# Optimization experiments

Hardware: AMD Instinct MI355X
Metric: run time of the kernel (lower is better)

The kernel has to match this reference:

```python
import jax, jax.numpy as jnp
import numpy as np

# CODABlocks (codomain attention) with per_channel_attention=True:
# token_codimension = head_codimension = 1, scale = 2, n_modes = [32, 32],
# mixer_modes = [16, 16], temperature = 1.0, instance_norm (affine) everywhere.
N_HEADS = 16
TEMPERATURE = 1.0
EPS = 1e-5

def _gelu(z):
    return jax.nn.gelu(z, approximate=False)  # matches torch F.gelu default (erf)

def instance_norm(x, g, b):
    # x: (B, C, H, W); normalize over spatial dims per (sample, channel), affine.
    mu = jnp.mean(x, axis=(-2, -1), keepdims=True)
    var = jnp.var(x, axis=(-2, -1), keepdims=True)
    return (x - mu) * jax.lax.rsqrt(var + EPS) * g[:, None, None] + b[:, None, None]

def conv1x1(x, w, b):
    return jnp.einsum('bihw,io->bohw', x, w) + b[None, :, None, None]

def fourier_resample(x, out_shape):
    # FFT-based spatial resampling (mode truncation / zero-pad), norm='forward'.
    if tuple(x.shape[-2:]) == tuple(out_shape):
        return x
    Ho, Wo = out_shape
    xft = jnp.fft.rfftn(x, axes=(-2, -1), norm='forward')
    out = jnp.zeros(x.shape[:-2] + (Ho, Wo // 2 + 1), dtype=xft.dtype)
    hk = min(x.shape[-2], Ho) // 2
    wk = min(xft.shape[-1], Wo // 2 + 1)
    out = out.at[..., :hk, :wk].set(xft[..., :hk, :wk])
    out = out.at[..., -hk:, :wk].set(xft[..., -hk:, :wk])
    return jnp.fft.irfftn(out, s=out_shape, axes=(-2, -1), norm='forward')

def spectral_conv(x, w, out_shape):
    # Truncated-mode spectral convolution (dense weights, equiv. to tucker rank=1.0).
    # w: (Cin, Cout, 2*mh, mw, 2) -> complex weight on kept Fourier modes.
    wc = w[..., 0] + 1j * w[..., 1]
    mh = wc.shape[2] // 2
    mw = wc.shape[3]
    Ho, Wo = out_shape
    xft = jnp.fft.rfftn(x, axes=(-2, -1), norm='forward')   # (B, Cin, H, W//2+1)
    top = jnp.einsum('bihw,iohw->bohw', xft[:, :, :mh, :mw], wc[:, :, :mh])
    bot = jnp.einsum('bihw,iohw->bohw', xft[:, :, -mh:, :mw], wc[:, :, mh:])
    out_ft = jnp.zeros((x.shape[0], wc.shape[1], Ho, Wo // 2 + 1), dtype=xft.dtype)
    out_ft = out_ft.at[:, :, :mh, :mw].set(top)
    out_ft = out_ft.at[:, :, -mh:, :mw].set(bot)
    return jnp.fft.irfftn(out_ft, s=out_shape, axes=(-2, -1), norm='forward')

def fno_layer(x, spec_w, skip_w, skip_b, out_shape, norm=None, act=None):
    # One FNOBlocks layer: spectral conv + (resampled) linear skip, optional norm/act.
    xs = fourier_resample(conv1x1(x, skip_w, skip_b), out_shape)
    xf = spectral_conv(x, spec_w, out_shape)
    if norm is not None:
        xf = instance_norm(xf, *norm)
    y = xf + xs
    return act(y) if act is not None else y

def codano_forward(x, key_w, key_skip_w, key_skip_b, query_w, query_skip_w, query_skip_b, value_w, value_skip_w, value_skip_b, proj_w, proj_skip_w, proj_skip_b, norm1_g, norm1_b, attn_norm_g, attn_norm_b, norm2_g, norm2_b, mixer_w1, mixer_skip_w1, mixer_skip_b1, mixer_norm_g1, mixer_norm_b1, mixer_w2, mixer_skip_w2, mixer_skip_b2, mixer_norm_g2, mixer_norm_b2, mixer_out_g, mixer_out_b):
    b, t, H, W = x.shape   # token codim d = 1 -> channel dim == number of tokens
    tokens = x.reshape(b * t, 1, H, W)
    tokens_norm = instance_norm(tokens, norm1_g, norm1_b)
    Hs, Ws = H // 2, W // 2   # K, Q downsampled by scale = 2
    k = fno_layer(tokens_norm, key_w, key_skip_w, key_skip_b, (Hs, Ws))
    q = fno_layer(tokens_norm, query_w, query_skip_w, query_skip_b, (Hs, Ws))
    v = fno_layer(tokens_norm, value_w, value_skip_w, value_skip_b, (H, W))

    def heads_flat(z):
        hh, ww = z.shape[-2:]
        # (b*t, n_heads*d, h, w) -> (b, heads, t, d*h*w), d = 1
        return z.reshape(b, t, N_HEADS, hh * ww).transpose(0, 2, 1, 3)

    kf, qf, vf = heads_flat(k), heads_flat(q), heads_flat(v)
    scale = jnp.sqrt(jnp.asarray(kf.shape[-1], jnp.float32)) * TEMPERATURE
    dprod = jax.nn.softmax(jnp.einsum('bhtd,bhsd->bhts', qf, kf) / scale, axis=-1)
    attn = jnp.einsum('bhts,bhsd->bhtd', dprod, vf)      # (b, heads, t, H*W)
    attn = attn.transpose(0, 2, 1, 3).reshape(b * t, N_HEADS, H, W)
    # multi-head projection back to token codimension (n_heads -> 1)
    attn = fno_layer(attn, proj_w, proj_skip_w, proj_skip_b, (H, W))
    attn = instance_norm(attn + tokens, attn_norm_g, attn_norm_b)
    # permutation-equivariant mixer: 2 FNO layers shared across all tokens
    m = instance_norm(attn, norm2_g, norm2_b)
    m = fno_layer(m, mixer_w1, mixer_skip_w1, mixer_skip_b1, (H, W), norm=(mixer_norm_g1, mixer_norm_b1), act=_gelu)
    m = fno_layer(m, mixer_w2, mixer_skip_w2, mixer_skip_b2, (H, W), norm=(mixer_norm_g2, mixer_norm_b2))
    out = instance_norm(m, mixer_out_g, mixer_out_b) + attn
    return out.reshape(b, t, H, W)

def setup_inputs():
    key = jax.random.key(0)
    ks = list(jax.random.split(key, 32))
    f32 = jnp.float32
    def W_(k, shape, s=0.02):
        return (s * jax.random.normal(k, shape)).astype(f32)
    B, T, H, Wd = 4, 32, 128, 128
    mh_s, mw_s = 16, 9    # mixer_modes [16,16]: 2*(16//2) rows, 16//2+1 rfft cols
    mh_f, mw_f = 32, 17   # n_modes [32,32]
    return {
        'x': jax.random.normal(ks[0], (B, T, H, Wd), dtype=f32),
        'key_w': W_(ks[1], (1, N_HEADS, mh_s, mw_s, 2)),
        'key_skip_w': W_(ks[2], (1, N_HEADS), 0.5),
        'key_skip_b': W_(ks[3], (N_HEADS,)),
        'query_w': W_(ks[4], (1, N_HEADS, mh_s, mw_s, 2)),
        'query_skip_w': W_(ks[5], (1, N_HEADS), 0.5),
        'query_skip_b': W_(ks[6], (N_HEADS,)),
        'value_w': W_(ks[7], (1, N_HEADS, mh_s, mw_s, 2)),
        'value_skip_w': W_(ks[8], (1, N_HEADS), 0.5),
        'value_skip_b': W_(ks[9], (N_HEADS,)),
        'proj_w': W_(ks[10], (N_HEADS, 1, mh_f, mw_f, 2)),
        'proj_skip_w': W_(ks[11], (N_HEADS, 1), 0.25),
        'proj_skip_b': W_(ks[12], (1,)),
        'norm1_g': jnp.ones((1,), f32), 'norm1_b': jnp.zeros((1,), f32),
        'attn_norm_g': jnp.ones((1,), f32), 'attn_norm_b': jnp.zeros((1,), f32),
        'norm2_g': jnp.ones((1,), f32), 'norm2_b': jnp.zeros((1,), f32),
        'mixer_w1': W_(ks[13], (1, 1, mh_f, mw_f, 2)),
        'mixer_skip_w1': W_(ks[14], (1, 1), 0.5),
        'mixer_skip_b1': W_(ks[15], (1,)),
        'mixer_norm_g1': jnp.ones((1,), f32), 'mixer_norm_b1': jnp.zeros((1,), f32),
        'mixer_w2': W_(ks[16], (1, 1, mh_f, mw_f, 2)),
        'mixer_skip_w2': W_(ks[17], (1, 1), 0.5),
        'mixer_skip_b2': W_(ks[18], (1,)),
        'mixer_norm_g2': jnp.ones((1,), f32), 'mixer_norm_b2': jnp.zeros((1,), f32),
        'mixer_out_g': jnp.ones((1,), f32), 'mixer_out_b': jnp.zeros((1,), f32),
    }

def reference(x, key_w, key_skip_w, key_skip_b, query_w, query_skip_w, query_skip_b, value_w, value_skip_w, value_skip_b, proj_w, proj_skip_w, proj_skip_b, norm1_g, norm1_b, attn_norm_g, attn_norm_b, norm2_g, norm2_b, mixer_w1, mixer_skip_w1, mixer_skip_b1, mixer_norm_g1, mixer_norm_b1, mixer_w2, mixer_skip_w2, mixer_skip_b2, mixer_norm_g2, mixer_norm_b2, mixer_out_g, mixer_out_b):
    return codano_forward(x, key_w, key_skip_w, key_skip_b, query_w, query_skip_w, query_skip_b, value_w, value_skip_w, value_skip_b, proj_w, proj_skip_w, proj_skip_b, norm1_g, norm1_b, attn_norm_g, attn_norm_b, norm2_g, norm2_b, mixer_w1, mixer_skip_w1, mixer_skip_b1, mixer_norm_g1, mixer_norm_b1, mixer_w2, mixer_skip_w2, mixer_skip_b2, mixer_norm_g2, mixer_norm_b2, mixer_out_g, mixer_out_b)
```

## Files before the change

### kernel.cpp

```cpp
#include <hip/hip_runtime.h>
#include <cmath>

#define PI_F 3.14159265358979323846f
#define NTOK 128
#define NPIX 16384
#define NHEADS 16

__device__ __forceinline__ void block_reduce2(float& a, float& b){
  __shared__ float sa[4], sb[4];
  __syncthreads();
  for (int o=32;o>0;o>>=1){ a += __shfl_down(a,o); b += __shfl_down(b,o); }
  int w = threadIdx.x>>6, l = threadIdx.x&63;
  if (l==0){ sa[w]=a; sb[w]=b; }
  __syncthreads();
  a = sa[0]+sa[1]+sa[2]+sa[3];
  b = sb[0]+sb[1]+sb[2]+sb[3];
}

__device__ __forceinline__ float block_reduce1(float a){
  __shared__ float sa[4];
  __syncthreads();
  for (int o=32;o>0;o>>=1) a += __shfl_down(a,o);
  int w = threadIdx.x>>6, l = threadIdx.x&63;
  if (l==0) sa[w]=a;
  __syncthreads();
  return sa[0]+sa[1]+sa[2]+sa[3];
}

__device__ __forceinline__ float gelu_f(float y){
  return 0.5f*y*(1.f + erff(y*0.70710678118f));
}

__device__ __forceinline__ void affine_from(const float* __restrict__ ps, float g, float bb, int t,
                                            float& a, float& b0){
  float sum=0.f,sq=0.f;
  #pragma unroll
  for (int s=0;s<8;s++){ const float* p=ps+((size_t)t*8+s)*2; sum+=p[0]; sq+=p[1]; }
  const float iN=1.f/NPIX;
  float mu=sum*iN, var=sq*iN-mu*mu;
  a=rsqrtf(var+1e-5f)*g;
  b0=bb-mu*a;
}
__device__ __forceinline__ void scalA_from(const float* __restrict__ psA, float ag, float n2g, int t,
                                           float& muZ, float& aA, float& a0){
  float sum=0.f,sq=0.f;
  #pragma unroll
  for (int s=0;s<16;s++){ const float* p=psA+((size_t)t*16+s)*2; sum+=p[0]; sq+=p[1]; }
  const float iN=1.f/NPIX;
  muZ=sum*iN; float var=sq*iN-muZ*muZ;
  float inv=rsqrtf(var+1e-5f);
  aA=inv*ag;
  float var2=aA*aA*var;
  a0=aA*rsqrtf(var2+1e-5f)*n2g;
}
__device__ __forceinline__ void scalB_from(const float* __restrict__ psB, float mng1, int t,
                                           float& mu1, float& c1){
  float sum=0.f,sq=0.f;
  #pragma unroll
  for (int s=0;s<16;s++){ const float* p=psB+((size_t)t*16+s)*2; sum+=p[0]; sq+=p[1]; }
  const float iN=1.f/NPIX;
  mu1=sum*iN; float var=sq*iN-mu1*mu1;
  c1=rsqrtf(var+1e-5f)*mng1;
}
__device__ __forceinline__ void scalC_from(const float* __restrict__ psC, float mng2, float K, float sw,
                                           float outg, int t,
                                           float& mu2f, float& c2, float& mu3, float& c3){
  float sf=0.f,sfsq=0.f,sm=0.f,smsq=0.f,sx=0.f;
  #pragma unroll
  for (int s=0;s<16;s++){
    const float* p=psC+((size_t)t*16+s)*5;
    sf+=p[0]; sfsq+=p[1]; sm+=p[2]; smsq+=p[3]; sx+=p[4];
  }
  const float iN=1.f/NPIX;
  mu2f=sf*iN; float var2=sfsq*iN-mu2f*mu2f;
  c2=rsqrtf(var2+1e-5f)*mng2;
  float Em1=sm*iN, Em1sq=smsq*iN, Exm=sx*iN;
  float Em2=K+sw*Em1;
  float Em2sq = c2*c2*var2 + sw*sw*Em1sq + K*K
              + 2.f*c2*sw*(Exm - mu2f*Em1) + 2.f*K*sw*Em1;
  float var_m2=Em2sq-Em2*Em2;
  mu3=Em2;
  c3=rsqrtf(var_m2+1e-5f)*outg;
}

__global__ __launch_bounds__(256) void k_scol(const float* __restrict__ x,
                        float* __restrict__ A, float* __restrict__ pstat){
  int bx=blockIdx.x;
  if (bx<1024){
    __shared__ float rows[2048];
    __shared__ float S1[2592];
    __shared__ float tw[256];
    int base = bx*16;
    for (int i=threadIdx.x;i<2048;i+=256) rows[i] = x[(size_t)base*128 + i];
    for (int p=threadIdx.x;p<128;p+=256){ float sn,cs; sincosf(-(2.f*PI_F/128.f)*(float)p,&sn,&cs); tw[p*2]=cs; tw[p*2+1]=sn; }
    __syncthreads();
    for (int e=threadIdx.x;e<1280;e+=256){
      int r=e/80, q=e%80, w0=q/5, k=q%5;
      const float* y=rows+r*128+w0;
      float re=0.f, im=0.f;
      #pragma unroll
      for (int w1=0;w1<8;w1++){
        int p=(16*k*w1)&127;
        float v=y[w1*16];
        re+=v*tw[p*2]; im+=v*tw[p*2+1];
      }
      float* o=S1+r*162+q*2; o[0]=re; o[1]=im;
    }
    __syncthreads();
    for (int e=threadIdx.x;e<528;e+=256){
      int r=e/33, c=e%33;
      int m=c&7; int ks=m; float sg=1.f;
      if (m>4){ ks=8-m; sg=-1.f; }
      const float* Sp=S1+r*162+ks*2;
      float re=0.f, im=0.f;
      #pragma unroll
      for (int w0=0;w0<16;w0++){
        int p=(c*w0)&127;
        float cr=tw[p*2], ci=tw[p*2+1];
        float sr=Sp[w0*10], si=sg*Sp[w0*10+1];
        re += sr*cr - si*ci;
        im += sr*ci + si*cr;
      }
      float* o=A+((size_t)(base+r)*33+c)*2; o[0]=re; o[1]=im;
    }
  } else {
    int u=bx-1024; int t=u>>3, slab=u&7;
    const float* xs = x + (size_t)t*NPIX + slab*2048;
    float sum=0.f, sq=0.f;
    for (int i=threadIdx.x;i<2048;i+=256){ float v=xs[i]; sum+=v; sq+=v*v; }
    block_reduce2(sum,sq);
    if (threadIdx.x==0){ float* o=pstat+((size_t)t*8+slab)*2; o[0]=sum; o[1]=sq; }
  }
}

__global__ __launch_bounds__(256) void k_rowfft64(const float* __restrict__ A,
                          const float* __restrict__ pstat0,
                          const float* __restrict__ n1g, const float* __restrict__ n1b,
                          float* __restrict__ X64, float* __restrict__ X64h){
  int s=blockIdx.x, cg2=blockIdx.y;
  int c0=cg2*11;
  __shared__ float a[128*11*2];
  __shared__ float S1[11*290];
  __shared__ float S[64][11][2];
  __shared__ float tw[128][2];
  for (int i=threadIdx.x;i<128*22;i+=256){
    int r=i/22, q=i%22;
    a[(r*11+(q>>1))*2+(q&1)] = A[((size_t)(s*128+r)*33 + c0)*2 + q];
// ... 104 lines not shown
          ppy = wp2[0]*x2i + wp2[1]*x2r;
        }
        Vx = 0.5f*(prx + ppx);
        Vy = 0.5f*(pry - ppy);
      }
      float xmr, xmi;
      if (c==0){ xmr=xh0[j].x; xmi=xh0[j].y; }
      else { xmr=Xs[(jj*17+c)*2]; xmi=Xs[(jj*17+c)*2+1]; }
      float zr = a*xmr + Vx;
      float zi = a*xmi + Vy;
      float wf = (side && c!=0)? 2.f : 1.f;
      float* dst = (side? Zk : Zq) + ((size_t)(t*16+h))*306 + m*2;
      dst[0]=wf*zr; dst[1]=wf*zi;
    }
    int b=t>>5, s=t&31;
    float vw=vsw[h], vb=vsb[h], pw=psw[h];
    size_t obase = ((size_t)(b*16+h)*32 + s)*1088;
    for (int e=threadIdx.x;e<544;e+=256){
      int j=e/17, c=e%17;
      float xr=Xs[e*2], xi=Xs[e*2+1];
      float wvr=0.f,wvi=0.f;
      if (c<=8 && (j<8||j>=24)){
        int jw=(j<8)? j : (j-16);
        const float* wv = value_w + ((size_t)(h*16+jw)*9 + c)*2;
        wvr=wv[0]; wvi=wv[1];
      }
      float Mr=xr*wvr-xi*wvi, Mi=xr*wvi+xi*wvr;
      float Mhr=Mr, Mhi=Mi;
      if (c==0){
        float Pr2=0.f,Pi2=0.f;
        int jp2=(j==0)?0:((j==16)?-1:32-j);
        if (jp2>=0 && (jp2<8||jp2>=24)){
          int jw2=(jp2<8)? jp2 : (jp2-16);
          const float* wv2=value_w+((size_t)(h*16+jw2)*9)*2;
          float pxr=Xs[(jp2*17)*2], pxi=Xs[(jp2*17)*2+1];
          Pr2=pxr*wv2[0]-pxi*wv2[1];
          Pi2=pxr*wv2[1]+pxi*wv2[0];
        }
        Mhr=0.5f*(Mr+Pr2); Mhi=0.5f*(Mi-Pi2);
      }
      float Yr=vw*xr+Mhr+((e==0)? vb:0.f);
      float Yi=vw*xi+Mhi;
      const float* pc=proj_w+((size_t)(h*32+j)*17+c)*2;
      float pr=pc[0], pi=pc[1];
      float* o=Yw+obase+e*2;
      o[0]=pr*Yr-pi*Yi+pw*Mr;
      o[1]=pr*Yi+pi*Yr+pw*Mi;
    }
  } else {
    int u=bx-2048;
    int b=u>>8, rem=u&255, t=rem>>3, sg=rem&7;
    float2* xt=(float2*)sh;
    const float2* src = (const float2*)(X64h + ((size_t)(b*32+t))*4224);
    for (int m=threadIdx.x;m<2112;m+=256){
      int r=m/33, c=m%33;
      bool excl = (c<=8) && (r<=8 || r>=56);
      float w = excl? 0.f : ((c==0||c==32)? 1.f : 2.f);
// ... 145 lines not shown
        const float* __restrict__ P, const float* __restrict__ X64,
        const float* __restrict__ pstat0,
        const float* __restrict__ n1g, const float* __restrict__ n1b,
        const float* __restrict__ pw, const float* __restrict__ vw,
        const float* __restrict__ psw, const float* __restrict__ vsb, const float* __restrict__ psb,
        float* __restrict__ zf, float* __restrict__ pstatA, float* __restrict__ sp){
  __shared__ float sh[1616];
  int bx=blockIdx.x;
  if (bx<2048){
    int bt=bx>>4, slab=bx&15;
    float* Ss=sh; float* T=sh+1088; float* tw=sh+1360;
    for (int i=threadIdx.x;i<1088;i+=256){
      const float* sp4 = Sfp + (size_t)bt*4352 + i;
      Ss[i] = sp4[0]+sp4[1088]+sp4[2176]+sp4[3264];
    }
    for (int p=threadIdx.x;p<128;p+=256){ float sn,cs; sincosf((2.f*PI_F/128.f)*(float)p,&sn,&cs); tw[p*2]=cs; tw[p*2+1]=sn; }
    __syncthreads();
    int h0 = slab*8;
    for (int e=threadIdx.x;e<136;e+=256){
      int hl=e/17, c=e%17; int h=h0+hl;
      float re=0.f, im=0.f;
      for (int j=0;j<32;j++){
        int r=(j<16)? j : (j+96);
        int p=(r*h)&127;
        float cs=tw[p*2], sn=tw[p*2+1];
        float ar=Ss[(j*17+c)*2], ai=Ss[(j*17+c)*2+1];
        re += ar*cs - ai*sn;
        im += ar*sn + ai*cs;
      }
      T[e*2]=re; T[e*2+1]=im;
    }
    __syncthreads();
    size_t base = (size_t)bt*NPIX + h0*128;
    float Cb = psb[0];
    for (int hh=0;hh<16;hh++) Cb += psw[hh]*vsb[hh];
    float sum=0.f, sq=0.f;
    for (int pos=threadIdx.x;pos<1024;pos+=256){
      int hl=pos>>7, w=pos&127;
      const float* Th=T+hl*17*2;
      float br=tw[w*2], bi=tw[w*2+1];
      float rr=br, ri=bi;
      float v=Th[0];
      for (int c=1;c<17;c++){
        v += 2.f*(Th[c*2]*rr - Th[c*2+1]*ri);
        float nr=rr*br-ri*bi; ri=rr*bi+ri*br; rr=nr;
      }
      float val = v + sk[base+pos] + x[base+pos] + Cb;
      zf[base+pos]=val; sum+=val; sq+=val*val;
    }
    block_reduce2(sum,sq);
    if (threadIdx.x==0){ float* o=pstatA+((size_t)bt*16+slab)*2; o[0]=sum; o[1]=sq; }
  } else {
    int u=bx-2048;
    int bt=u>>1, ec=u&1; int b=bt>>5, t=bt&31;
    float* Sfl=sh; float* Rs=sh+1088;
    if (threadIdx.x<32){
      int s=threadIdx.x; float acc=0.f;
      for (int h=0;h<16;h++)
        acc += pw[h]*vw[h]*P[(((size_t)(b*16+h)*32)+t)*32+s];
      Rs[s]=acc;
    }
// ... 20 lines not shown
      const float* xb = X64 + ((size_t)(b*32)*(64*33) + i2*33 + c)*2;
      for (int s=0;s<32;s++){
        const float* xp = xb + (size_t)s*(64*33)*2;
        float r=Rs[s];
        re += r*xp[0]; im += r*xp[1];
      }
      const float* xt = X64 + ((size_t)bt*(64*33) + i2*33 + c)*2;
      re += inva*xt[0]; im += inva*xt[1];
      float zr=sr+re, zi=si+im;
      if (e==0) zr += Cb - b0_t*inva;
      sp[((size_t)bt*544+e)*2]=zr; sp[((size_t)bt*544+e)*2+1]=zi;
    }
  }
}

__global__ __launch_bounds__(256) void k_field1(const float* __restrict__ sp, const float* __restrict__ wm,
        const float* __restrict__ pstatA,
        const float* __restrict__ ag, const float* __restrict__ n2g, const float* __restrict__ n2b,
        float* __restrict__ fd1, float* __restrict__ pstatB){
  int bt = blockIdx.x, slab = blockIdx.y;
  __shared__ float Ss[1088];
  __shared__ float T[8*17*2];
  __shared__ float tw[128][2];
  float muZ,aA,a0;
  scalA_from(pstatA, ag[0], n2g[0], bt, muZ, aA, a0);
  float d0 = n2b[0] - muZ*a0;
  for (int e=threadIdx.x;e<544;e+=256){
    float xr=a0*sp[((size_t)bt*544+e)*2] + ((e==0)? d0 : 0.f);
    float xi=a0*sp[((size_t)bt*544+e)*2+1];
    float wr=wm[e*2], wi=wm[e*2+1];
    Ss[e*2]=xr*wr-xi*wi; Ss[e*2+1]=xr*wi+xi*wr;
  }
  for (int p=threadIdx.x;p<128;p+=256){ float sn,cs; sincosf((2.f*PI_F/128.f)*(float)p,&sn,&cs); tw[p][0]=cs; tw[p][1]=sn; }
  __syncthreads();
  int h0 = slab*8;
  for (int e=threadIdx.x;e<8*17;e+=256){
    int hl=e/17, c=e%17; int h=h0+hl;
    float re=0.f, im=0.f;
    for (int j=0;j<32;j++){
      int r=(j<16)? j : (j+96);
      int p=(r*h)&127;
      float cs=tw[p][0], sn=tw[p][1];
      float ar=Ss[(j*17+c)*2], ai=Ss[(j*17+c)*2+1];
      re += ar*cs - ai*sn;
      im += ar*sn + ai*cs;
    }
    T[e*2]=re; T[e*2+1]=im;
  }
  __syncthreads();
  size_t base = (size_t)bt*NPIX + h0*128;
  float sum=0.f, sq=0.f;
  for (int pos=threadIdx.x;pos<1024;pos+=256){
    int hl=pos>>7, w=pos&127;
    const float* Th=T+hl*17*2;
    float br=tw[w][0], bi=tw[w][1];
    float rr=br, ri=bi;
    float v=Th[0];
    for (int c=1;c<17;c++){
      v += 2.f*(Th[c*2]*rr - Th[c*2+1]*ri);
      float nr=rr*br-ri*bi; ri=rr*bi+ri*br; rr=nr;
    }
    fd1[base+pos]=v; sum+=v; sq+=v*v;
  }
  block_reduce2(sum,sq);
  if (threadIdx.x==0){ float* o=pstatB+((size_t)bt*16+slab)*2; o[0]=sum; o[1]=sq; }
}

__global__ __launch_bounds__(256) void k_colA1(const float* __restrict__ f1, const float* __restrict__ z,
        const float* __restrict__ pstatA, const float* __restrict__ pstatB,
        const float* __restrict__ ag, const float* __restrict__ n2g, const float* __restrict__ mng1,
        const float* __restrict__ n2b,
        const float* __restrict__ mnb1, const float* __restrict__ msw1, const float* __restrict__ msb1,
        float* __restrict__ A){
  __shared__ float rows[16*128];
  __shared__ float S1[2592];
  __shared__ float tw[128][2];
  int grow = blockIdx.x*16;
  int t = grow>>7;
  float muZ,aA,a0;
  scalA_from(pstatA, ag[0], n2g[0], t, muZ, aA, a0);
  float b2 = n2b[0];
  float mu1,c1;
  scalB_from(pstatB, mng1[0], t, mu1, c1);
  float nb=mnb1[0], sw=msw1[0], sb=msb1[0];
  for (int i=threadIdx.x;i<2048;i+=256){
    size_t gi=(size_t)grow*128+i;
    float m0v=(z[gi]-muZ)*a0+b2;
    float y=(f1[gi]-mu1)*c1+nb + m0v*sw + sb;
    rows[i]=gelu_f(y);
  }
  for (int p=threadIdx.x;p<128;p+=256){ float sn,cs; sincosf(-(2.f*PI_F/128.f)*(float)p,&sn,&cs); tw[p][0]=cs; tw[p][1]=sn; }
  __syncthreads();
  for (int e=threadIdx.x;e<1280;e+=256){
    int r=e/80, q=e%80, w0=q/5, k=q%5;
    const float* y=rows+r*128+w0;
    float re=0.f, im=0.f;
    #pragma unroll
    for (int w1=0;w1<8;w1++){
      int p=(16*k*w1)&127;
      float v=y[w1*16];
      re+=v*tw[p][0]; im+=v*tw[p][1];
    }
    float* o=S1+r*162+q*2; o[0]=re; o[1]=im;
  }
  __syncthreads();
  for (int e=threadIdx.x;e<272;e+=256){
    int r=e/17, c=e%17;
    int m=c&7; int ks=m; float sg=1.f;
    if (m>4){ ks=8-m; sg=-1.f; }
    const float* Sp=S1+r*162+ks*2;
    float re=0.f, im=0.f;
    #pragma unroll
    for (int w0=0;w0<16;w0++){
      int p=(c*w0)&127;
      float cr=tw[p][0], ci=tw[p][1];
      float sr=Sp[w0*10], si=sg*Sp[w0*10+1];
      re += sr*cr - si*ci;
      im += sr*ci + si*cr;
    }
    float* o=A+((size_t)(grow+r)*17+c)*2; o[0]=re; o[1]=im;
  }
}

__global__ __launch_bounds__(256) void k_rowfft32(const float* __restrict__ A, float* __restrict__ spec){
  int s=blockIdx.x, cg2=blockIdx.y;
  int c0 = (cg2==0)? 0 : (1+cg2*4);
  int nc = (cg2==0)? 5 : 4;
  __shared__ float a[128*5*2];
  __shared__ float tw[128][2];
  for (int i=threadIdx.x;i<128*nc*2;i+=256){
    int r=i/(2*nc), q=i%(2*nc);
    a[(r*5+(q>>1))*2+(q&1)] = A[((size_t)(s*128+r)*17 + c0)*2 + q];
  }
  for (int p=threadIdx.x;p<128;p+=256){ float sn,cs; sincosf(-(2.f*PI_F/128.f)*(float)p,&sn,&cs); tw[p][0]=cs; tw[p][1]=sn; }
  __syncthreads();
  const float sc=1.f/16384.f;
  for (int e=threadIdx.x;e<32*nc;e+=256){
    int j=e/nc, cl=e%nc;
    int r=(j<16)? j : (j+96);
    float re=0.f,im=0.f;
    for (int h=0;h<128;h++){
      int p=(r*h)&127;
      float cs=tw[p][0], sn=tw[p][1];
      float ar=a[(h*5+cl)*2], ai=a[(h*5+cl)*2+1];
      re += ar*cs - ai*sn;
      im += ar*sn + ai*cs;
    }
    float* o=spec+((size_t)s*544 + j*17 + c0+cl)*2;
    o[0]=re*sc; o[1]=im*sc;
  }
}

__global__ __launch_bounds__(256) void k_field2(const float* __restrict__ sp2, const float* __restrict__ wm,
        const float* __restrict__ f1, const float* __restrict__ z,
        const float* __restrict__ pstatA, const float* __restrict__ pstatB,
        const float* __restrict__ ag, const float* __restrict__ n2g, const float* __restrict__ mng1,
        const float* __restrict__ n2b, const float* __restrict__ mnb1,
        const float* __restrict__ msw1, const float* __restrict__ msb1,
        float* __restrict__ fd2, float* __restrict__ pstatC){
  int bt = blockIdx.x, slab = blockIdx.y;
  __shared__ float Ss[1088];
  __shared__ float T[8*17*2];
  __shared__ float tw[128][2];
  for (int e=threadIdx.x;e<544;e+=256){
    float xr=sp2[((size_t)bt*544+e)*2], xi=sp2[((size_t)bt*544+e)*2+1];
    float wr=wm[e*2], wi=wm[e*2+1];
    Ss[e*2]=xr*wr-xi*wi; Ss[e*2+1]=xr*wi+xi*wr;
  }
  for (int p=threadIdx.x;p<128;p+=256){ float sn,cs; sincosf((2.f*PI_F/128.f)*(float)p,&sn,&cs); tw[p][0]=cs; tw[p][1]=sn; }
  __syncthreads();
  int h0 = slab*8;
  for (int e=threadIdx.x;e<8*17;e+=256){
    int hl=e/17, c=e%17; int h=h0+hl;
    float re=0.f, im=0.f;
    for (int j=0;j<32;j++){
      int r=(j<16)? j : (j+96);
      int p=(r*h)&127;
      float cs=tw[p][0], sn=tw[p][1];
      float ar=Ss[(j*17+c)*2], ai=Ss[(j*17+c)*2+1];
      re += ar*cs - ai*sn;
      im += ar*sn + ai*cs;
    }
    T[e*2]=re; T[e*2+1]=im;
  }
  __syncthreads();
  size_t base = (size_t)bt*NPIX + h0*128;
  float muZ,aA,a0,mu1,c1;
  scalA_from(pstatA, ag[0], n2g[0], bt, muZ, aA, a0);
  scalB_from(pstatB, mng1[0], bt, mu1, c1);
  float b2=n2b[0], nb1=mnb1[0], sw1=msw1[0], sb1=msb1[0];
  float s_f=0.f,s_fsq=0.f,s_m=0.f,s_msq=0.f,s_x=0.f;
  for (int pos=threadIdx.x;pos<1024;pos+=256){
    int hl=pos>>7, w=pos&127;
    const float* Th=T+hl*17*2;
    float br=tw[w][0], bi=tw[w][1];
    float rr=br, ri=bi;
    float v=Th[0];
    for (int c=1;c<17;c++){
      v += 2.f*(Th[c*2]*rr - Th[c*2+1]*ri);
      float nr=rr*br-ri*bi; ri=rr*bi+ri*br; rr=nr;
    }
    size_t gi=base+pos;
    float m0v=(z[gi]-muZ)*a0+b2;
    float y=(f1[gi]-mu1)*c1+nb1 + m0v*sw1 + sb1;
    float m1v=gelu_f(y);
    fd2[gi]=v;
    s_f+=v; s_fsq+=v*v; s_m+=m1v; s_msq+=m1v*m1v; s_x+=v*m1v;
  }
  block_reduce2(s_f,s_fsq);
  block_reduce2(s_m,s_msq);
  s_x = block_reduce1(s_x);
  if (threadIdx.x==0){
    float* o=pstatC+((size_t)bt*16+slab)*5;
    o[0]=s_f; o[1]=s_fsq; o[2]=s_m; o[3]=s_msq; o[4]=s_x;
  }
}

__global__ __launch_bounds__(256) void k_final2(const float* __restrict__ z, const float* __restrict__ f1,
        const float* __restrict__ f2,
        const float* __restrict__ pstatA, const float* __restrict__ pstatB, const float* __restrict__ pstatC,
        const float* __restrict__ ag, const float* __restrict__ n2g, const float* __restrict__ mng1,
        const float* __restrict__ mng2, const float* __restrict__ outg,
        const float* __restrict__ ab, const float* __restrict__ n2b,
        const float* __restrict__ mnb1, const float* __restrict__ msw1, const float* __restrict__ msb1,
        const float* __restrict__ mnb2, const float* __restrict__ msw2, const float* __restrict__ msb2,
        const float* __restrict__ outb, float* __restrict__ out){
  int bt=blockIdx.x, slab=blockIdx.y;
  float muZ,aA,a0,mu1,c1,mu2f,c2,mu3,c3;
  scalA_from(pstatA, ag[0], n2g[0], bt, muZ, aA, a0);
  scalB_from(pstatB, mng1[0], bt, mu1, c1);
  float sw2=msw2[0], K=mnb2[0]+msb2[0];
  scalC_from(pstatC, mng2[0], K, sw2, outg[0], bt, mu2f, c2, mu3, c3);
  float b1=ab[0], b2=n2b[0], nb1=mnb1[0], sw1=msw1[0], sb1=msb1[0];
  float nb2=mnb2[0], sb2=msb2[0], bo=outb[0];
  size_t base=(size_t)bt*NPIX + (size_t)slab*1024;
  for (int i=threadIdx.x;i<1024;i+=256){
    size_t gi=base+i;
    float zv=z[gi];
    float m0v=(zv-muZ)*a0+b2;
    float a2v=(zv-muZ)*aA+b1;
    float y=(f1[gi]-mu1)*c1+nb1 + m0v*sw1 + sb1;
    float m1v=gelu_f(y);
    float m2v=(f2[gi]-mu2f)*c2+nb2 + m1v*sw2 + sb2;
    out[gi]=(m2v-mu3)*c3+bo+a2v;
  }
}

extern "C" void kernel_launch(void* const* d_in, const int* in_sizes, int n_in,
                              void* d_out, int out_size, void* d_ws, size_t ws_size,
                              hipStream_t stream){
  const float* x        = (const float*)d_in[0];
  const float* key_w    = (const float*)d_in[1];
  const float* key_sw   = (const float*)d_in[2];
  const float* key_sb   = (const float*)d_in[3];
  const float* query_w  = (const float*)d_in[4];
  const float* query_sw = (const float*)d_in[5];
  const float* query_sb = (const float*)d_in[6];
  const float* value_w  = (const float*)d_in[7];
// ... 23 lines not shown
  float* out = (float*)d_out;
  float* ws  = (float*)d_ws;

  size_t off=0;
  float* A   = ws + off; off += (size_t)128*128*33*2;
  float* X64 = ws + off; off += (size_t)128*64*33*2;
  float* X64h= ws + off; off += (size_t)128*64*33*2;
  float* Zq  = ws + off; off += (size_t)128*16*306;
  float* Zk  = ws + off; off += (size_t)128*16*306;
  float* Ue  = ws + off; off += (size_t)4*32*32;
  float* P   = ws + off; off += (size_t)4*16*32*32;
  float* Yw  = ws + off; off += (size_t)2048*1088;
  float* Sfp = ws + off; off += (size_t)128*4*1088;
  float* sk  = ws + off; off += (size_t)128*16384;
  float* zf  = ws + off; off += (size_t)128*16384;
  float* fd1 = ws + off; off += (size_t)128*16384;
  float* fd2 = ws + off; off += (size_t)128*16384;
  float* sp  = ws + off; off += (size_t)128*544*2;
  float* sp2 = ws + off; off += (size_t)128*544*2;
  float* pstat0 = ws + off; off += (size_t)128*8*2;
  float* pstatA = ws + off; off += (size_t)128*16*2;
  float* pstatB = ws + off; off += (size_t)128*16*2;
  float* pstatC = ws + off; off += (size_t)128*16*5;

  k_scol<<<2048,256,0,stream>>>(x, A, pstat0);
  k_rowfft64<<<dim3(128,3),256,0,stream>>>(A, pstat0, norm1_g, norm1_b, X64, X64h);
  k_UeZYw<<<3072,256,0,stream>>>(X64, X64h, query_w, query_sw, key_w, key_sw,
      value_w, value_sw, value_sb, proj_w, proj_sw, Zq, Zk, Yw, Ue);
  k_scores2<<<dim3(4,16,2),256,0,stream>>>(Zq, Zk, Ue, query_sw, query_sb, key_sw, key_sb, P);
  k_SfSk<<<528,256,0,stream>>>(x, P, Yw, proj_sw, value_sw, pstat0, norm1_g, norm1_b, Sfp, sk);
  k_f0sp<<<2304,256,0,stream>>>(Sfp, sk, x, P, X64, pstat0, norm1_g, norm1_b,
      proj_sw, value_sw, proj_sw, value_sb, proj_sb, zf, pstatA, sp);
  k_field1<<<dim3(128,16),256,0,stream>>>(sp, mw1, pstatA, attn_g, norm2_g, norm2_b, fd1, pstatB);
  k_colA1<<<1024,256,0,stream>>>(fd1, zf, pstatA, pstatB, attn_g, norm2_g, mng1,
      norm2_b, mnb1, msw1, msb1, A);
  k_rowfft32<<<dim3(128,4),256,0,stream>>>(A, sp2);
  k_field2<<<dim3(128,16),256,0,stream>>>(sp2, mw2, fd1, zf, pstatA, pstatB,
      attn_g, norm2_g, mng1, norm2_b, mnb1, msw1, msb1, fd2, pstatC);
  k_final2<<<dim3(128,16),256,0,stream>>>(zf, fd1, fd2, pstatA, pstatB, pstatC,
      attn_g, norm2_g, mng1, mng2, outg, attn_b, norm2_b,
      mnb1, msw1, msb1, mnb2, msw2, msb2, outb, out);
}
```

Baseline: 274.3 us.

## Fuse mixer tail into one per-sample kernel and merge stats into k_scol

The five tail kernels (field1, colA1, rowfft32, field2, final2) are replaced by a single k_tail kernel with one 1024-thread block per token. That block keeps the full 128x128 mixer field in LDS and computes instance-norm statistics with in-block reductions instead of global partial stats. This removes the fd1/fd2/sp2 global round trips, several launches, and the gelu recomputation. k_scol now computes the input stats alongside the column DFT instead of in separate blocks, and the inverse row DFT uses precomputed per-thread twiddles instead of a recurrence. The cost is that only 128 large blocks run, which limits occupancy on the tail, and the tail's column transform runs serially over 8 chunks.

```diff
diff --git a/kernel.cpp b/kernel.cpp
--- a/kernel.cpp
+++ b/kernel.cpp
@@ -25,6 +25,21 @@
   if (l==0) sa[w]=a;
   __syncthreads();
   return sa[0]+sa[1]+sa[2]+sa[3];
+}
+
+__device__ __forceinline__ float br1k(float a, float* scr){
+  __syncthreads();
+  for (int o=32;o>0;o>>=1) a += __shfl_down(a,o);
+  int w=threadIdx.x>>6, l=threadIdx.x&63;
+  if (l==0) scr[w]=a;
+  __syncthreads();
+  if (threadIdx.x<64){
+    float v=(threadIdx.x<16)? scr[threadIdx.x] : 0.f;
+    for (int o=8;o>0;o>>=1) v += __shfl_down(v,o);
+    if (threadIdx.x==0) scr[16]=v;
+  }
+  __syncthreads();
+  return scr[16];
 }
 
 __device__ __forceinline__ float gelu_f(float y){
@@ -53,84 +68,52 @@
   float var2=aA*aA*var;
   a0=aA*rsqrtf(var2+1e-5f)*n2g;
 }
-__device__ __forceinline__ void scalB_from(const float* __restrict__ psB, float mng1, int t,
-                                           float& mu1, float& c1){
-  float sum=0.f,sq=0.f;
-  #pragma unroll
-  for (int s=0;s<16;s++){ const float* p=psB+((size_t)t*16+s)*2; sum+=p[0]; sq+=p[1]; }
-  const float iN=1.f/NPIX;
-  mu1=sum*iN; float var=sq*iN-mu1*mu1;
-  c1=rsqrtf(var+1e-5f)*mng1;
-}
-__device__ __forceinline__ void scalC_from(const float* __restrict__ psC, float mng2, float K, float sw,
-                                           float outg, int t,
-                                           float& mu2f, float& c2, float& mu3, float& c3){
-  float sf=0.f,sfsq=0.f,sm=0.f,smsq=0.f,sx=0.f;
-  #pragma unroll
-  for (int s=0;s<16;s++){
-    const float* p=psC+((size_t)t*16+s)*5;
-    sf+=p[0]; sfsq+=p[1]; sm+=p[2]; smsq+=p[3]; sx+=p[4];
-  }
-  const float iN=1.f/NPIX;
-  mu2f=sf*iN; float var2=sfsq*iN-mu2f*mu2f;
-  c2=rsqrtf(var2+1e-5f)*mng2;
-  float Em1=sm*iN, Em1sq=smsq*iN, Exm=sx*iN;
-  float Em2=K+sw*Em1;
-  float Em2sq = c2*c2*var2 + sw*sw*Em1sq + K*K
-              + 2.f*c2*sw*(Exm - mu2f*Em1) + 2.f*K*sw*Em1;
-  float var_m2=Em2sq-Em2*Em2;
-  mu3=Em2;
-  c3=rsqrtf(var_m2+1e-5f)*outg;
-}
 
 __global__ __launch_bounds__(256) void k_scol(const float* __restrict__ x,
                         float* __restrict__ A, float* __restrict__ pstat){
+  __shared__ float rows[2048];
+  __shared__ float S1[2592];
+  __shared__ float tw[256];
   int bx=blockIdx.x;
-  if (bx<1024){
-    __shared__ float rows[2048];
-    __shared__ float S1[2592];
-    __shared__ float tw[256];
-    int base = bx*16;
-    for (int i=threadIdx.x;i<2048;i+=256) rows[i] = x[(size_t)base*128 + i];
-    for (int p=threadIdx.x;p<128;p+=256){ float sn,cs; sincosf(-(2.f*PI_F/128.f)*(float)p,&sn,&cs); tw[p*2]=cs; tw[p*2+1]=sn; }
-    __syncthreads();
-    for (int e=threadIdx.x;e<1280;e+=256){
-      int r=e/80, q=e%80, w0=q/5, k=q%5;
-      const float* y=rows+r*128+w0;
-      float re=0.f, im=0.f;
-      #pragma unroll
-      for (int w1=0;w1<8;w1++){
-        int p=(16*k*w1)&127;
-        float v=y[w1*16];
-        re+=v*tw[p*2]; im+=v*tw[p*2+1];
-      }
-      float* o=S1+r*162+q*2; o[0]=re; o[1]=im;
-    }
-    __syncthreads();
-    for (int e=threadIdx.x;e<528;e+=256){
-      int r=e/33, c=e%33;
-      int m=c&7; int ks=m; float sg=1.f;
-      if (m>4){ ks=8-m; sg=-1.f; }
-      const float* Sp=S1+r*162+ks*2;
-      float re=0.f, im=0.f;
-      #pragma unroll
-      for (int w0=0;w0<16;w0++){
-        int p=(c*w0)&127;
-        float cr=tw[p*2], ci=tw[p*2+1];
-        float sr=Sp[w0*10], si=sg*Sp[w0*10+1];
-        re += sr*cr - si*ci;
-        im += sr*ci + si*cr;
-      }
-      float* o=A+((size_t)(base+r)*33+c)*2; o[0]=re; o[1]=im;
-    }
-  } else {
-    int u=bx-1024; int t=u>>3, slab=u&7;
-    const float* xs = x + (size_t)t*NPIX + slab*2048;
-    float sum=0.f, sq=0.f;
-    for (int i=threadIdx.x;i<2048;i+=256){ float v=xs[i]; sum+=v; sq+=v*v; }
-    block_reduce2(sum,sq);
-    if (threadIdx.x==0){ float* o=pstat+((size_t)t*8+slab)*2; o[0]=sum; o[1]=sq; }
-  }
+  int base = bx*16;
+  float sum=0.f, sq=0.f;
+  for (int i=threadIdx.x;i<2048;i+=256){
+    float v = x[(size_t)base*128 + i];
+    rows[i]=v; sum+=v; sq+=v*v;
+  }
+  for (int p=threadIdx.x;p<128;p+=256){ float sn,cs; sincosf(-(2.f*PI_F/128.f)*(float)p,&sn,&cs); tw[p*2]=cs; tw[p*2+1]=sn; }
+  __syncthreads();
+  for (int e=threadIdx.x;e<1280;e+=256){
+    int r=e/80, q=e%80, w0=q/5, k=q%5;
+    const float* y=rows+r*128+w0;
+    float re=0.f, im=0.f;
+    #pragma unroll
+    for (int w1=0;w1<8;w1++){
+      int p=(16*k*w1)&127;
+      float v=y[w1*16];
+      re+=v*tw[p*2]; im+=v*tw[p*2+1];
+    }
+    float* o=S1+r*162+q*2; o[0]=re; o[1]=im;
+  }
+  __syncthreads();
+  for (int e=threadIdx.x;e<528;e+=256){
+    int r=e/33, c=e%33;
+    int m=c&7; int ks=m; float sg=1.f;
+    if (m>4){ ks=8-m; sg=-1.f; }
+    const float* Sp=S1+r*162+ks*2;
+    float re=0.f, im=0.f;
+    #pragma unroll
+    for (int w0=0;w0<16;w0++){
+      int p=(c*w0)&127;
+      float cr=tw[p*2], ci=tw[p*2+1];
+      float sr=Sp[w0*10], si=sg*Sp[w0*10+1];
+      re += sr*cr - si*ci;
+      im += sr*ci + si*cr;
+    }
+    float* o=A+((size_t)(base+r)*33+c)*2; o[0]=re; o[1]=im;
+  }
+  block_reduce2(sum,sq);
+  if (threadIdx.x==0){ float* o=pstat+(size_t)bx*2; o[0]=sum; o[1]=sq; }
 }
 
 __global__ __launch_bounds__(256) void k_rowfft64(const float* __restrict__ A,
@@ -265,7 +248,7 @@
       dst[0]=wf*zr; dst[1]=wf*zi;
     }
     int b=t>>5, s=t&31;
-    float vw=vsw[h], vb=vsb[h], pw=psw[h];
+    float vw_=vsw[h], vb=vsb[h], pw=psw[h];
     size_t obase = ((size_t)(b*16+h)*32 + s)*1088;
     for (int e=threadIdx.x;e<544;e+=256){
       int j=e/17, c=e%17;
@@ -290,8 +273,8 @@
         }
         Mhr=0.5f*(Mr+Pr2); Mhi=0.5f*(Mi-Pi2);
       }
-      float Yr=vw*xr+Mhr+((e==0)? vb:0.f);
-      float Yi=vw*xi+Mhi;
+      float Yr=vw_*xr+Mhr+((e==0)? vb:0.f);
+      float Yi=vw_*xi+Mhi;
       const float* pc=proj_w+((size_t)(h*32+j)*17+c)*2;
       float pr=pc[0], pi=pc[1];
       float* o=Yw+obase+e*2;
@@ -467,7 +450,7 @@
       const float* sp4 = Sfp + (size_t)bt*4352 + i;
       Ss[i] = sp4[0]+sp4[1088]+sp4[2176]+sp4[3264];
     }
-    for (int p=threadIdx.x;p<128;p+=256){ float sn,cs; sincosf((2.f*PI_F/128.f)*(float)p,&sn,&cs); tw[p*2]=cs; tw[p*2+1]=sn; }
+    for (int q=threadIdx.x;q<128;q+=256){ float sn,cs; sincosf((2.f*PI_F/128.f)*(float)q,&sn,&cs); tw[q*2]=cs; tw[q*2+1]=sn; }
     __syncthreads();
     int h0 = slab*8;
     for (int e=threadIdx.x;e<136;e+=256){
@@ -487,17 +470,19 @@
     size_t base = (size_t)bt*NPIX + h0*128;
     float Cb = psb[0];
     for (int hh=0;hh<16;hh++) Cb += psw[hh]*vsb[hh];
+    int w=threadIdx.x&127, hl0=threadIdx.x>>7;
+    float cw[16], swt[16];
+    #pragma unroll
+    for (int c=0;c<16;c++){ int p=((c+1)*w)&127; cw[c]=tw[p*2]; swt[c]=tw[p*2+1]; }
     float sum=0.f, sq=0.f;
-    for (int pos=threadIdx.x;pos<1024;pos+=256){
-      int hl=pos>>7, w=pos&127;
-      const float* Th=T+hl*17*2;
-      float br=tw[w*2], bi=tw[w*2+1];
-      float rr=br, ri=bi;
-      float v=Th[0];
-      for (int c=1;c<17;c++){
-        v += 2.f*(Th[c*2]*rr - Th[c*2+1]*ri);
-        float nr=rr*br-ri*bi; ri=rr*bi+ri*br; rr=nr;
-      }
+    #pragma unroll
+    for (int pp=0;pp<4;pp++){
+      int hl=hl0+2*pp;
+      const float2* Th=(const float2*)(T+hl*34);
+      float v=Th[0].x;
+      #pragma unroll
+      for (int c=0;c<16;c++){ float2 th=Th[c+1]; v += 2.f*(th.x*cw[c] - th.y*swt[c]); }
+      int pos=hl*128+w;
       float val = v + sk[base+pos] + x[base+pos] + Cb;
       zf[base+pos]=val; sum+=val; sq+=val*val;
     }
@@ -548,234 +533,184 @@
   }
 }
 
-__global__ __launch_bounds__(256) void k_field1(const float* __restrict__ sp, const float* __restrict__ wm,
-        const float* __restrict__ pstatA,
-        const float* __restrict__ ag, const float* __restrict__ n2g, const float* __restrict__ n2b,
-        float* __restrict__ fd1, float* __restrict__ pstatB){
-  int bt = blockIdx.x, slab = blockIdx.y;
-  __shared__ float Ss[1088];
-  __shared__ float T[8*17*2];
-  __shared__ float tw[128][2];
+__global__ __launch_bounds__(1024,1) void k_tail(const float* __restrict__ sp,
+    const float* __restrict__ wm1, const float* __restrict__ wm2,
+    const float* __restrict__ zf, const float* __restrict__ pstatA,
+    const float* __restrict__ ag, const float* __restrict__ n2g, const float* __restrict__ n2b,
+    const float* __restrict__ mng1, const float* __restrict__ mnb1,
+    const float* __restrict__ msw1, const float* __restrict__ msb1,
+    const float* __restrict__ mng2, const float* __restrict__ mnb2,
+    const float* __restrict__ msw2, const float* __restrict__ msb2,
+    const float* __restrict__ ab, const float* __restrict__ outg, const float* __restrict__ outb,
+    float* __restrict__ out){
+  __shared__ float T1A[4352];
+  __shared__ float T2[4352];
+  __shared__ float m1s[16384];
+  __shared__ float S1[2592];
+  __shared__ float spb[1088];
+  __shared__ float tw[256];
+  __shared__ float red[20];
+  int bt=blockIdx.x, tid=threadIdx.x;
   float muZ,aA,a0;
   scalA_from(pstatA, ag[0], n2g[0], bt, muZ, aA, a0);
-  float d0 = n2b[0] - muZ*a0;
-  for (int e=threadIdx.x;e<544;e+=256){
-    float xr=a0*sp[((size_t)bt*544+e)*2] + ((e==0)? d0 : 0.f);
+  float b2=n2b[0];
+  float d0=b2 - muZ*a0;
+  for (int e=tid;e<544;e+=1024){
+    float xr=a0*sp[((size_t)bt*544+e)*2] + ((e==0)? d0:0.f);
     float xi=a0*sp[((size_t)bt*544+e)*2+1];
-    float wr=wm[e*2], wi=wm[e*2+1];
-    Ss[e*2]=xr*wr-xi*wi; Ss[e*2+1]=xr*wi+xi*wr;
-  }
-  for (int p=threadIdx.x;p<128;p+=256){ float sn,cs; sincosf((2.f*PI_F/128.f)*(float)p,&sn,&cs); tw[p][0]=cs; tw[p][1]=sn; }
-  __syncthreads();
-  int h0 = slab*8;
-  for (int e=threadIdx.x;e<8*17;e+=256){
-    int hl=e/17, c=e%17; int h=h0+hl;
+    float wr=wm1[e*2], wi=wm1[e*2+1];
+    spb[e*2]=xr*wr-xi*wi; spb[e*2+1]=xr*wi+xi*wr;
+  }
+  for (int p=tid;p<128;p+=1024){ float sn,cs; sincosf((2.f*PI_F/128.f)*(float)p,&sn,&cs); tw[p*2]=cs; tw[p*2+1]=sn; }
+  __syncthreads();
+  for (int e=tid;e<2176;e+=1024){
+    int h=e/17, c=e%17;
     float re=0.f, im=0.f;
     for (int j=0;j<32;j++){
       int r=(j<16)? j : (j+96);
       int p=(r*h)&127;
-      float cs=tw[p][0], sn=tw[p][1];
-      float ar=Ss[(j*17+c)*2], ai=Ss[(j*17+c)*2+1];
+      float cs=tw[p*2], sn=tw[p*2+1];
+      float ar=spb[(j*17+c)*2], ai=spb[(j*17+c)*2+1];
       re += ar*cs - ai*sn;
       im += ar*sn + ai*cs;
     }
-    T[e*2]=re; T[e*2+1]=im;
-  }
-  __syncthreads();
-  size_t base = (size_t)bt*NPIX + h0*128;
-  float sum=0.f, sq=0.f;
-  for (int pos=threadIdx.x;pos<1024;pos+=256){
-    int hl=pos>>7, w=pos&127;
-    const float* Th=T+hl*17*2;
-    float br=tw[w][0], bi=tw[w][1];
-    float rr=br, ri=bi;
+    T1A[e*2]=re; T1A[e*2+1]=im;
+  }
+  __syncthreads();
+  int w=tid&127, h0=tid>>7;
+  float cw[16], swt[16];
+  #pragma unroll
+  for (int c=0;c<16;c++){ int p=((c+1)*w)&127; cw[c]=tw[p*2]; swt[c]=tw[p*2+1]; }
+  float sum1=0.f, sq1=0.f;
+  for (int p=0;p<16;p++){
+    int h=h0+8*p;
+    const float* Th=T1A+h*34;
     float v=Th[0];
-    for (int c=1;c<17;c++){
-      v += 2.f*(Th[c*2]*rr - Th[c*2+1]*ri);
-      float nr=rr*br-ri*bi; ri=rr*bi+ri*br; rr=nr;
-    }
-    fd1[base+pos]=v; sum+=v; sq+=v*v;
-  }
-  block_reduce2(sum,sq);
-  if (threadIdx.x==0){ float* o=pstatB+((size_t)bt*16+slab)*2; o[0]=sum; o[1]=sq; }
-}
-
-__global__ __launch_bounds__(256) void k_colA1(const float* __restrict__ f1, const float* __restrict__ z,
-        const float* __restrict__ pstatA, const float* __restrict__ pstatB,
-        const float* __restrict__ ag, const float* __restrict__ n2g, const float* __restrict__ mng1,
-        const float* __restrict__ n2b,
-        const float* __restrict__ mnb1, const float* __restrict__ msw1, const float* __restrict__ msb1,
-        float* __restrict__ A){
-  __shared__ float rows[16*128];
-  __shared__ float S1[2592];
-  __shared__ float tw[128][2];
-  int grow = blockIdx.x*16;
-  int t = grow>>7;
-  float muZ,aA,a0;
-  scalA_from(pstatA, ag[0], n2g[0], t, muZ, aA, a0);
-  float b2 = n2b[0];
-  float mu1,c1;
-  scalB_from(pstatB, mng1[0], t, mu1, c1);
-  float nb=mnb1[0], sw=msw1[0], sb=msb1[0];
-  for (int i=threadIdx.x;i<2048;i+=256){
-    size_t gi=(size_t)grow*128+i;
-    float m0v=(z[gi]-muZ)*a0+b2;
-    float y=(f1[gi]-mu1)*c1+nb + m0v*sw + sb;
-    rows[i]=gelu_f(y);
-  }
-  for (int p=threadIdx.x;p<128;p+=256){ float sn,cs; sincosf(-(2.f*PI_F/128.f)*(float)p,&sn,&cs); tw[p][0]=cs; tw[p][1]=sn; }
-  __syncthreads();
-  for (int e=threadIdx.x;e<1280;e+=256){
-    int r=e/80, q=e%80, w0=q/5, k=q%5;
-    const float* y=rows+r*128+w0;
+    #pragma unroll
+    for (int c=0;c<16;c++){ v += 2.f*(Th[(c+1)*2]*cw[c] - Th[(c+1)*2+1]*swt[c]); }
+    m1s[h*128+w]=v; sum1+=v; sq1+=v*v;
+  }
+  float S1s=br1k(sum1,red);
+  float Q1s=br1k(sq1,red);
+  const float iN=1.f/16384.f;
+  float mu1=S1s*iN;
+  float var1=Q1s*iN - mu1*mu1;
+  float c1=rsqrtf(var1+1e-5f)*mng1[0];
+  float nb1=mnb1[0], sw1=msw1[0], sb1=msb1[0];
+  size_t base=(size_t)bt*NPIX;
+  for (int p=0;p<16;p++){
+    int h=h0+8*p;
+    int idx=h*128+w;
+    size_t gi=base+idx;
+    float m0v=(zf[gi]-muZ)*a0+b2;
+    float y=(m1s[idx]-mu1)*c1+nb1 + m0v*sw1 + sb1;
+    m1s[idx]=gelu_f(y);
+  }
+  __syncthreads();
+  for (int chn=0; chn<8; chn++){
+    int grow=chn*16;
+    for (int e=tid;e<1280;e+=1024){
+      int r=e/80, q=e%80, w0=q/5, k=q%5;
+      const float* y=m1s+(grow+r)*128+w0;
+      float re=0.f, im=0.f;
+      #pragma unroll
+      for (int w1=0;w1<8;w1++){
+        int p=(16*k*w1)&127;
+        float v=y[w1*16];
+        re += v*tw[p*2];
+        im -= v*tw[p*2+1];
+      }
+      float* o=S1+r*162+q*2; o[0]=re; o[1]=im;
+    }
+    __syncthreads();
+    for (int e=tid;e<272;e+=1024){
+      int r=e/17, c=e%17;
+      int m=c&7, ks=m; float sg=1.f;
+      if (m>4){ ks=8-m; sg=-1.f; }
+      const float* Sp=S1+r*162+ks*2;
+      float re=0.f, im=0.f;
+      #pragma unroll
+      for (int w0=0;w0<16;w0++){
+        int p=(c*w0)&127;
+        float cs=tw[p*2], sn=tw[p*2+1];
+        float sr=Sp[w0*10], si=sg*Sp[w0*10+1];
+        re += sr*cs + si*sn;
+        im += -sr*sn + si*cs;
+      }
+      T1A[((grow+r)*17+c)*2]=re; T1A[((grow+r)*17+c)*2+1]=im;
+    }
+    __syncthreads();
+  }
+  const float sc=1.f/16384.f;
+  for (int e=tid;e<544;e+=1024){
+    int j=e/17, c=e%17;
+    int r=(j<16)? j : (j+96);
     float re=0.f, im=0.f;
-    #pragma unroll
-    for (int w1=0;w1<8;w1++){
-      int p=(16*k*w1)&127;
-      float v=y[w1*16];
-      re+=v*tw[p][0]; im+=v*tw[p][1];
-    }
-    float* o=S1+r*162+q*2; o[0]=re; o[1]=im;
-  }
-  __syncthreads();
-  for (int e=threadIdx.x;e<272;e+=256){
-    int r=e/17, c=e%17;
-    int m=c&7; int ks=m; float sg=1.f;
-    if (m>4){ ks=8-m; sg=-1.f; }
-    const float* Sp=S1+r*162+ks*2;
-    float re=0.f, im=0.f;
-    #pragma unroll
-    for (int w0=0;w0<16;w0++){
-      int p=(c*w0)&127;
-      float cr=tw[p][0], ci=tw[p][1];
-      float sr=Sp[w0*10], si=sg*Sp[w0*10+1];
-      re += sr*cr - si*ci;
-      im += sr*ci + si*cr;
-    }
-    float* o=A+((size_t)(grow+r)*17+c)*2; o[0]=re; o[1]=im;
-  }
-}
-
-__global__ __launch_bounds__(256) void k_rowfft32(const float* __restrict__ A, float* __restrict__ spec){
-  int s=blockIdx.x, cg2=blockIdx.y;
-  int c0 = (cg2==0)? 0 : (1+cg2*4);
-  int nc = (cg2==0)? 5 : 4;
-  __shared__ float a[128*5*2];
-  __shared__ float tw[128][2];
-  for (int i=threadIdx.x;i<128*nc*2;i+=256){
-    int r=i/(2*nc), q=i%(2*nc);
-    a[(r*5+(q>>1))*2+(q&1)] = A[((size_t)(s*128+r)*17 + c0)*2 + q];
-  }
-  for (int p=threadIdx.x;p<128;p+=256){ float sn,cs; sincosf(-(2.f*PI_F/128.f)*(float)p,&sn,&cs); tw[p][0]=cs; tw[p][1]=sn; }
-  __syncthreads();
-  const float sc=1.f/16384.f;
-  for (int e=threadIdx.x;e<32*nc;e+=256){
-    int j=e/nc, cl=e%nc;
-    int r=(j<16)? j : (j+96);
-    float re=0.f,im=0.f;
     for (int h=0;h<128;h++){
       int p=(r*h)&127;
-      float cs=tw[p][0], sn=tw[p][1];
-      float ar=a[(h*5+cl)*2], ai=a[(h*5+cl)*2+1];
-      re += ar*cs - ai*sn;
-      im += ar*sn + ai*cs;
-    }
-    float* o=spec+((size_t)s*544 + j*17 + c0+cl)*2;
-    o[0]=re*sc; o[1]=im*sc;
-  }
-}
-
-__global__ __launch_bounds__(256) void k_field2(const float* __restrict__ sp2, const float* __restrict__ wm,
-        const float* __restrict__ f1, const float* __restrict__ z,
-        const float* __restrict__ pstatA, const float* __restrict__ pstatB,
-        const float* __restrict__ ag, const float* __restrict__ n2g, const float* __restrict__ mng1,
-        const float* __restrict__ n2b, const float* __restrict__ mnb1,
-        const float* __restrict__ msw1, const float* __restrict__ msb1,
-        float* __restrict__ fd2, float* __restrict__ pstatC){
-  int bt = blockIdx.x, slab = blockIdx.y;
-  __shared__ float Ss[1088];
-  __shared__ float T[8*17*2];
-  __shared__ float tw[128][2];
-  for (int e=threadIdx.x;e<544;e+=256){
-    float xr=sp2[((size_t)bt*544+e)*2], xi=sp2[((size_t)bt*544+e)*2+1];
-    float wr=wm[e*2], wi=wm[e*2+1];
-    Ss[e*2]=xr*wr-xi*wi; Ss[e*2+1]=xr*wi+xi*wr;
-  }
-  for (int p=threadIdx.x;p<128;p+=256){ float sn,cs; sincosf((2.f*PI_F/128.f)*(float)p,&sn,&cs); tw[p][0]=cs; tw[p][1]=sn; }
-  __syncthreads();
-  int h0 = slab*8;
-  for (int e=threadIdx.x;e<8*17;e+=256){
-    int hl=e/17, c=e%17; int h=h0+hl;
+      float cs=tw[p*2], sn=tw[p*2+1];
+      float ar=T1A[(h*17+c)*2], ai=T1A[(h*17+c)*2+1];
+      re += ar*cs + ai*sn;
+      im += -ar*sn + ai*cs;
+    }
+    spb[e*2]=re*sc; spb[e*2+1]=im*sc;
+  }
+  __syncthreads();
+  for (int e=tid;e<544;e+=1024){
+    float xr=spb[e*2], xi=spb[e*2+1];
+    float wr=wm2[e*2], wi=wm2[e*2+1];
+    spb[e*2]=xr*wr-xi*wi; spb[e*2+1]=xr*wi+xi*wr;
+  }
+  __syncthreads();
+  for (int e=tid;e<2176;e+=1024){
+    int h=e/17, c=e%17;
     float re=0.f, im=0.f;
     for (int j=0;j<32;j++){
       int r=(j<16)? j : (j+96);
       int p=(r*h)&127;
-      float cs=tw[p][0], sn=tw[p][1];
-      float ar=Ss[(j*17+c)*2], ai=Ss[(j*17+c)*2+1];
+      float cs=tw[p*2], sn=tw[p*2+1];
+      float ar=spb[(j*17+c)*2], ai=spb[(j*17+c)*2+1];
       re += ar*cs - ai*sn;
       im += ar*sn + ai*cs;
     }
-    T[e*2]=re; T[e*2+1]=im;
-  }
-  __syncthreads();
-  size_t base = (size_t)bt*NPIX + h0*128;
-  float muZ,aA,a0,mu1,c1;
-  scalA_from(pstatA, ag[0], n2g[0], bt, muZ, aA, a0);
-  scalB_from(pstatB, mng1[0], bt, mu1, c1);
-  float b2=n2b[0], nb1=mnb1[0], sw1=msw1[0], sb1=msb1[0];
-  float s_f=0.f,s_fsq=0.f,s_m=0.f,s_msq=0.f,s_x=0.f;
-  for (int pos=threadIdx.x;pos<1024;pos+=256){
-    int hl=pos>>7, w=pos&127;
-    const float* Th=T+hl*17*2;
-    float br=tw[w][0], bi=tw[w][1];
-    float rr=br, ri=bi;
+    T2[e*2]=re; T2[e*2+1]=im;
+  }
+  __syncthreads();
+  float s_f=0.f, s_fsq=0.f, s_m=0.f, s_msq=0.f, s_x=0.f;
+  for (int p=0;p<16;p++){
+    int h=h0+8*p;
+    const float* Th=T2+h*34;
     float v=Th[0];
-    for (int c=1;c<17;c++){
-      v += 2.f*(Th[c*2]*rr - Th[c*2+1]*ri);
-      float nr=rr*br-ri*bi; ri=rr*bi+ri*br; rr=nr;
-    }
-    size_t gi=base+pos;
-    float m0v=(z[gi]-muZ)*a0+b2;
-    float y=(f1[gi]-mu1)*c1+nb1 + m0v*sw1 + sb1;
-    float m1v=gelu_f(y);
-    fd2[gi]=v;
+    #pragma unroll
+    for (int c=0;c<16;c++){ v += 2.f*(Th[(c+1)*2]*cw[c] - Th[(c+1)*2+1]*swt[c]); }
+    float m1v=m1s[h*128+w];
     s_f+=v; s_fsq+=v*v; s_m+=m1v; s_msq+=m1v*m1v; s_x+=v*m1v;
   }
-  block_reduce2(s_f,s_fsq);
-  block_reduce2(s_m,s_msq);
-  s_x = block_reduce1(s_x);
-  if (threadIdx.x==0){
-    float* o=pstatC+((size_t)bt*16+slab)*5;
-    o[0]=s_f; o[1]=s_fsq; o[2]=s_m; o[3]=s_msq; o[4]=s_x;
-  }
-}
-
-__global__ __launch_bounds__(256) void k_final2(const float* __restrict__ z, const float* __restrict__ f1,
-        const float* __restrict__ f2,
-        const float* __restrict__ pstatA, const float* __restrict__ pstatB, const float* __restrict__ pstatC,
-        const float* __restrict__ ag, const float* __restrict__ n2g, const float* __restrict__ mng1,
-        const float* __restrict__ mng2, const float* __restrict__ outg,
-        const float* __restrict__ ab, const float* __restrict__ n2b,
-        const float* __restrict__ mnb1, const float* __restrict__ msw1, const float* __restrict__ msb1,
-        const float* __restrict__ mnb2, const float* __restrict__ msw2, const float* __restrict__ msb2,
-        const float* __restrict__ outb, float* __restrict__ out){
-  int bt=blockIdx.x, slab=blockIdx.y;
-  float muZ,aA,a0,mu1,c1,mu2f,c2,mu3,c3;
-  scalA_from(pstatA, ag[0], n2g[0], bt, muZ, aA, a0);
-  scalB_from(pstatB, mng1[0], bt, mu1, c1);
-  float sw2=msw2[0], K=mnb2[0]+msb2[0];
-  scalC_from(pstatC, mng2[0], K, sw2, outg[0], bt, mu2f, c2, mu3, c3);
-  float b1=ab[0], b2=n2b[0], nb1=mnb1[0], sw1=msw1[0], sb1=msb1[0];
-  float nb2=mnb2[0], sb2=msb2[0], bo=outb[0];
-  size_t base=(size_t)bt*NPIX + (size_t)slab*1024;
-  for (int i=threadIdx.x;i<1024;i+=256){
-    size_t gi=base+i;
-    float zv=z[gi];
-    float m0v=(zv-muZ)*a0+b2;
-    float a2v=(zv-muZ)*aA+b1;
-    float y=(f1[gi]-mu1)*c1+nb1 + m0v*sw1 + sb1;
-    float m1v=gelu_f(y);
-    float m2v=(f2[gi]-mu2f)*c2+nb2 + m1v*sw2 + sb2;
+  float Sf=br1k(s_f,red);
+  float Sfsq=br1k(s_fsq,red);
+  float Sm=br1k(s_m,red);
+  float Smsq=br1k(s_msq,red);
+  float Sx=br1k(s_x,red);
+  float mu2f=Sf*iN;
+  float var2=Sfsq*iN - mu2f*mu2f;
+  float c2=rsqrtf(var2+1e-5f)*mng2[0];
+  float Em1=Sm*iN, Em1sq=Smsq*iN, Exm=Sx*iN;
+  float K=mnb2[0]+msb2[0], sw2=msw2[0];
+  float Em2=K+sw2*Em1;
+  float Em2sq=c2*c2*var2 + sw2*sw2*Em1sq + K*K + 2.f*c2*sw2*(Exm-mu2f*Em1) + 2.f*K*sw2*Em1;
+  float mu3=Em2;
+  float c3=rsqrtf(Em2sq-Em2*Em2+1e-5f)*outg[0];
+  float b1=ab[0], nb2=mnb2[0], sb2=msb2[0], bo=outb[0];
+  for (int p=0;p<16;p++){
+    int h=h0+8*p;
+    const float* Th=T2+h*34;
+    float v=Th[0];
+    #pragma unroll
+    for (int c=0;c<16;c++){ v += 2.f*(Th[(c+1)*2]*cw[c] - Th[(c+1)*2+1]*swt[c]); }
+    size_t gi=base+(size_t)h*128+w;
+    float a2v=(zf[gi]-muZ)*aA+b1;
+    float m1v=m1s[h*128+w];
+    float m2v=(v-mu2f)*c2+nb2 + m1v*sw2 + sb2;
     out[gi]=(m2v-mu3)*c3+bo+a2v;
   }
 }
@@ -829,16 +764,11 @@
   float* Sfp = ws + off; off += (size_t)128*4*1088;
   float* sk  = ws + off; off += (size_t)128*16384;
   float* zf  = ws + off; off += (size_t)128*16384;
-  float* fd1 = ws + off; off += (size_t)128*16384;
-  float* fd2 = ws + off; off += (size_t)128*16384;
   float* sp  = ws + off; off += (size_t)128*544*2;
-  float* sp2 = ws + off; off += (size_t)128*544*2;
   float* pstat0 = ws + off; off += (size_t)128*8*2;
   float* pstatA = ws + off; off += (size_t)128*16*2;
-  float* pstatB = ws + off; off += (size_t)128*16*2;
-  float* pstatC = ws + off; off += (size_t)128*16*5;
-
-  k_scol<<<2048,256,0,stream>>>(x, A, pstat0);
+
+  k_scol<<<1024,256,0,stream>>>(x, A, pstat0);
   k_rowfft64<<<dim3(128,3),256,0,stream>>>(A, pstat0, norm1_g, norm1_b, X64, X64h);
   k_UeZYw<<<3072,256,0,stream>>>(X64, X64h, query_w, query_sw, key_w, key_sw,
       value_w, value_sw, value_sb, proj_w, proj_sw, Zq, Zk, Yw, Ue);
@@ -846,13 +776,7 @@
   k_SfSk<<<528,256,0,stream>>>(x, P, Yw, proj_sw, value_sw, pstat0, norm1_g, norm1_b, Sfp, sk);
   k_f0sp<<<2304,256,0,stream>>>(Sfp, sk, x, P, X64, pstat0, norm1_g, norm1_b,
       proj_sw, value_sw, proj_sw, value_sb, proj_sb, zf, pstatA, sp);
-  k_field1<<<dim3(128,16),256,0,stream>>>(sp, mw1, pstatA, attn_g, norm2_g, norm2_b, fd1, pstatB);
-  k_colA1<<<1024,256,0,stream>>>(fd1, zf, pstatA, pstatB, attn_g, norm2_g, mng1,
-      norm2_b, mnb1, msw1, msb1, A);
-  k_rowfft32<<<dim3(128,4),256,0,stream>>>(A, sp2);
-  k_field2<<<dim3(128,16),256,0,stream>>>(sp2, mw2, fd1, zf, pstatA, pstatB,
-      attn_g, norm2_g, mng1, norm2_b, mnb1, msw1, msb1, fd2, pstatC);
-  k_final2<<<dim3(128,16),256,0,stream>>>(zf, fd1, fd2, pstatA, pstatB, pstatC,
-      attn_g, norm2_g, mng1, mng2, outg, attn_b, norm2_b,
-      mnb1, msw1, msb1, mnb2, msw2, msb2, outb, out);
-}
+  k_tail<<<128,1024,0,stream>>>(sp, mw1, mw2, zf, pstatA,
+      attn_g, norm2_g, norm2_b, mng1, mnb1, msw1, msb1,
+      mng2, mnb2, msw2, msb2, attn_b, outg, outb, out);
+}
```

Result: no change. 277.8 us (+1.3%).
